# Kernel tuning notes

Hardware: AMD Instinct MI355X
Metric: run time of the kernel (lower is better)

## Reference

```python
import jax, jax.numpy as jnp
import numpy as np


def _gcn_conv(x, W, b, src, dst, n):
    # PyG GCNConv: add self-loops, symmetric normalization deg^{-1/2} A deg^{-1/2},
    # linear transform, scatter-add aggregation, bias.
    h = x @ W  # [N, H]
    # degree including self-loop (count of dst occurrences + 1)
    deg = jnp.zeros((n,), h.dtype).at[dst].add(1.0) + 1.0
    dinv = jax.lax.rsqrt(deg)  # deg^{-1/2}
    edge_norm = (dinv[src] * dinv[dst])[:, None]  # [E, 1]
    agg = jax.ops.segment_sum(h[src] * edge_norm, dst, num_segments=n)  # [N, H]
    # self-loop contribution: norm = dinv[i]*dinv[i]
    return agg + h * (dinv * dinv)[:, None] + b


def setup_inputs() -> dict:
    N, E, F_IN, HID, OUT = 100000, 1600000, 128, 128, 64
    key = jax.random.key(0)
    ks = jax.random.split(key, 8)
    x = jax.random.normal(ks[0], (N, F_IN), dtype=jnp.float32)
    edge_index = jax.random.randint(ks[1], (2, E), 0, N, dtype=jnp.int32)
    s1 = 1.0 / np.sqrt(F_IN)
    s2 = 1.0 / np.sqrt(HID)
    W1 = jax.random.uniform(ks[2], (F_IN, HID), jnp.float32, -s1, s1)
    b1 = jax.random.uniform(ks[3], (HID,), jnp.float32, -s1, s1)
    W2 = jax.random.uniform(ks[4], (HID, HID), jnp.float32, -s2, s2)
    b2 = jax.random.uniform(ks[5], (HID,), jnp.float32, -s2, s2)
    W_out = jax.random.uniform(ks[6], (HID, OUT), jnp.float32, -s2, s2)
    b_out = jax.random.uniform(ks[7], (OUT,), jnp.float32, -s2, s2)
    return {"x": x, "edge_index": edge_index, "W1": W1, "b1": b1,
            "W2": W2, "b2": b2, "W_out": W_out, "b_out": b_out}


def reference(x, edge_index, W1, b1, W2, b2, W_out, b_out):
    n = x.shape[0]
    src, dst = edge_index[0], edge_index[1]
    h = _gcn_conv(x, W1, b1, src, dst, n)
    h = jax.nn.relu(h)
    # F.dropout(training=self.training): identity in eval mode
    h = _gcn_conv(h, W2, b2, src, dst, n)
    h = jax.nn.relu(h)
    logits = h @ W_out + b_out
    return jax.nn.log_softmax(logits, axis=1)
```

## Files before the change

kernel.cpp:

```cpp
#include <hip/hip_runtime.h>
#include <hip/hip_bf16.h>


#define FEAT 128
#define OUTF 64
#define BSH 7
#define BNODES (1 << BSH)
#define SCHUNK_SH 12
#define SCHUNK (1 << SCHUNK_SH)
#define NREP 8
#define GDEPTH 16

typedef __attribute__((ext_vector_type(8))) short short8;
typedef __attribute__((ext_vector_type(4))) float f32x4;

__device__ __forceinline__ unsigned short bf16_rn(float f) {
    unsigned int u = __float_as_uint(f);
    u += 0x7FFFu + ((u >> 16) & 1u);
    return (unsigned short)(u >> 16);
}
__device__ __forceinline__ float bf16_lo(unsigned int u) { return __uint_as_float(u << 16); }
__device__ __forceinline__ float bf16_hi(unsigned int u) { return __uint_as_float(u & 0xFFFF0000u); }

__global__ __launch_bounds__(256) void bincount8_kernel(
        const int* __restrict__ dst, int* __restrict__ bcnt8, int E, int NB) {
    __shared__ int h[8192];
    int t = threadIdx.x;
    int nb8 = NB * NREP;
    for (int i = t; i < nb8; i += 256) h[i] = 0;
    __syncthreads();
    int stride = gridDim.x * 256;
    for (int e = blockIdx.x * 256 + t; e < E; e += stride) {
        int rep = (e >> SCHUNK_SH) & (NREP - 1);
        atomicAdd(&h[((dst[e] >> BSH) << 3) | rep], 1);
    }
    __syncthreads();
    for (int i = t; i < nb8; i += 256)
        if (h[i]) atomicAdd(&bcnt8[i], h[i]);
}

__global__ __launch_bounds__(1024) void bucket_scan8_kernel(
        const int* __restrict__ bcnt8, int* __restrict__ bcur8,
        int* __restrict__ bbase, int NB, int E) {
    int t = threadIdx.x;
    int nb8 = NB * NREP;
    int base = t * 8;
    int v[8];
    #pragma unroll
    for (int i = 0; i < 8; ++i) v[i] = (base + i < nb8) ? bcnt8[base + i] : 0;
    int local = 0;
    #pragma unroll
    for (int i = 0; i < 8; ++i) local += v[i];
    int lane = t & 63, wv = t >> 6;
    int x = local;
    #pragma unroll
    for (int o = 1; o < 64; o <<= 1) {
        int y = __shfl_up(x, o);
        if (lane >= o) x += y;
    }
    __shared__ int wsum[16];
    if (lane == 63) wsum[wv] = x;
    __syncthreads();
    int woff = 0;
    for (int i = 0; i < wv; ++i) woff += wsum[i];
    int run = woff + x - local;
    #pragma unroll
    for (int i = 0; i < 8; ++i) {
        int g = base + i;
        if (g < nb8) {
            bcur8[g] = run;
            if ((g & (NREP - 1)) == 0) bbase[g >> 3] = run;
        }
        run += v[i];
    }
    if (t == 0) bbase[NB] = E;
}

__global__ __launch_bounds__(256) void bin_scatter_kernel(
        const int* __restrict__ src, const int* __restrict__ dst,
        int* __restrict__ bcur8, unsigned int* __restrict__ staged,
        int E, int NB) {
    __shared__ int lcnt[1024];
    __shared__ int lbase[1024];
    int t = threadIdx.x;
    int rep = blockIdx.x & (NREP - 1);
    int e0 = blockIdx.x << SCHUNK_SH;
    int e1 = min(e0 + SCHUNK, E);
    for (int i = t; i < NB; i += 256) lcnt[i] = 0;
    __syncthreads();
    for (int e = e0 + t; e < e1; e += 256)
        atomicAdd(&lcnt[dst[e] >> BSH], 1);
    __syncthreads();
    for (int i = t; i < NB; i += 256) {
        int c = lcnt[i];
        lbase[i] = c ? atomicAdd(&bcur8[(i << 3) | rep], c) : 0;
        lcnt[i] = 0;
    }
    __syncthreads();
    for (int e = e0 + t; e < e1; e += 256) {
        int s = src[e], d = dst[e];
        int b = d >> BSH, dl = d & (BNODES - 1);
        int pos = lbase[b] + atomicAdd(&lcnt[b], 1);
        staged[pos] = (unsigned int)s | ((unsigned int)dl << 25);
    }
}

__global__ __launch_bounds__(256) void bucket_place_kernel(
        const unsigned int* __restrict__ staged, const int* __restrict__ bbase,
        int* __restrict__ row_ptr, float* __restrict__ dinv,
        int* __restrict__ csr_src, int N, int E) {
    int b = blockIdx.x;
    int t = threadIdx.x;
    int base = bbase[b], end = bbase[b + 1];
    __shared__ int cnt[BNODES];
    __shared__ int cur[BNODES];
    __shared__ int wsum2[2];
    if (t < BNODES) cnt[t] = 0;
    __syncthreads();
    for (int i = base + t; i < end; i += 256)
        atomicAdd(&cnt[staged[i] >> 25], 1);
    __syncthreads();

    bool act = t < BNODES;
    int v = act ? cnt[t] : 0;
    int lane = t & 63, wv = t >> 6;
    int x = v;
    #pragma unroll
    for (int o = 1; o < 64; o <<= 1) {
        int y = __shfl_up(x, o);
        if (lane >= o) x += y;
    }
    if (lane == 63 && wv == 0) wsum2[0] = x;
    __syncthreads();
    if (act) {
        int excl = x - v + (wv == 1 ? wsum2[0] : 0);
        int gnode = b * BNODES + t;
        int rp = base + excl;
        cur[t] = rp;
        if (gnode < N) {
            row_ptr[gnode] = rp;
            dinv[gnode] = rsqrtf((float)v + 1.0f);
        }
    }
    __syncthreads();
    for (int i = base + t; i < end; i += 256) {
        unsigned int u = staged[i];
        int dl = u >> 25;
        int p = atomicAdd(&cur[dl], 1);
        csr_src[p] = (int)(u & 0x1FFFFFFu);
    }
    if (b == 0 && t == 0) row_ptr[N] = E;
}

__global__ __launch_bounds__(256) void convw_kernel(
        const float* __restrict__ W1, const float* __restrict__ W2,
        const float* __restrict__ Wout,
        __hip_bfloat16* __restrict__ W1t, __hip_bfloat16* __restrict__ W2t,
        __hip_bfloat16* __restrict__ WoutT) {
    int idx = blockIdx.x * 256 + threadIdx.x;
    if (idx < 2 * FEAT * FEAT) {
        int which = idx >> 14;
        int r = idx & (FEAT * FEAT - 1);
        int n = r >> 7, k = r & 127;
        const float* W = which ? W2 : W1;
        unsigned short* Wt = (unsigned short*)(which ? W2t : W1t);
        Wt[r] = bf16_rn(W[k * FEAT + n]);
    } else if (idx < 2 * FEAT * FEAT + OUTF * FEAT) {
        int r = idx - 2 * FEAT * FEAT;
        int n = r >> 7, k = r & 127;
        ((unsigned short*)WoutT)[r] = bf16_rn(Wout[k * OUTF + n]);
    }
}

template <bool IN_FP32>
__global__ __launch_bounds__(256) void mfma_gemm_kernel(
        const void* __restrict__ Xv, const __hip_bfloat16* __restrict__ Wt,
        const float* __restrict__ dinv, __hip_bfloat16* __restrict__ Y, int N) {
    __shared__ short Ws[FEAT][136];
    int t = threadIdx.x;
    for (int i = t; i < FEAT * 16; i += 256) {
        int n = i >> 4, c = i & 15;
        *(uint4*)&Ws[n][c * 8] = *(const uint4*)((const unsigned short*)Wt + n * FEAT + c * 8);
    }
    __syncthreads();

    int wave = t >> 6, lane = t & 63;
    int m = lane & 15, quad = lane >> 4;
    int rbase = (blockIdx.x * 4 + wave) * 16;
    if (rbase >= N) return;
    int row = rbase + m;
    bool rok = row < N;

    f32x4 acc[8];
    #pragma unroll
    for (int nt = 0; nt < 8; ++nt) acc[nt] = (f32x4){0.f, 0.f, 0.f, 0.f};

    #pragma unroll
    for (int ks = 0; ks < 4; ++ks) {
        short8 a;
        if (IN_FP32) {
            const float* X = (const float*)Xv;
            float xs[8];
            if (rok) {
                float4 x0 = *(const float4*)(X + (size_t)row * FEAT + ks * 32 + quad * 8);
                float4 x1 = *(const float4*)(X + (size_t)row * FEAT + ks * 32 + quad * 8 + 4);
                xs[0] = x0.x; xs[1] = x0.y; xs[2] = x0.z; xs[3] = x0.w;
                xs[4] = x1.x; xs[5] = x1.y; xs[6] = x1.z; xs[7] = x1.w;
            } else {
                #pragma unroll
                for (int j = 0; j < 8; ++j) xs[j] = 0.f;
            }
            #pragma unroll
            for (int j = 0; j < 8; ++j) a[j] = (short)bf16_rn(xs[j]);
        } else {
            const unsigned short* X = (const unsigned short*)Xv;
            if (rok)
                a = *(const short8*)(X + (size_t)row * FEAT + ks * 32 + quad * 8);
            else {
                #pragma unroll
                for (int j = 0; j < 8; ++j) a[j] = 0;
            }
        }
        #pragma unroll
        for (int nt = 0; nt < 8; ++nt) {
            short8 bfr = *(const short8*)&Ws[nt * 16 + m][ks * 32 + quad * 8];
            acc[nt] = __builtin_amdgcn_mfma_f32_16x16x32_bf16(a, bfr, acc[nt], 0, 0, 0);
        }
    }

    float dr[4];
    #pragma unroll
    for (int r = 0; r < 4; ++r) {
        int ro = rbase + quad * 4 + r;
        dr[r] = (ro < N) ? dinv[ro] : 0.f;
    }
    unsigned short* Yo = (unsigned short*)Y;
    #pragma unroll
    for (int nt = 0; nt < 8; ++nt) {
        #pragma unroll
        for (int r = 0; r < 4; ++r) {
            int ro = rbase + quad * 4 + r;
            if (ro < N)
                Yo[(size_t)ro * FEAT + nt * 16 + m] = bf16_rn(acc[nt][r] * dr[r]);
        }
    }
}

template <int EPI>
__global__ __launch_bounds__(256, 4) void gather_fused_kernel(
        const int* __restrict__ row_ptr, const int* __restrict__ csr_src,
        const float* __restrict__ dinv, const __hip_bfloat16* __restrict__ Hs,
        const float* __restrict__ bias, const __hip_bfloat16* __restrict__ Wt,
        const float* __restrict__ bvec, void* __restrict__ outp, int N) {
    __shared__ short As[16][136];

    int t = threadIdx.x;
    int lane = t & 63;
    int wave = t >> 6;
    int grp = lane >> 4;
    int fl = lane & 15;
    int node = blockIdx.x * 16 + wave * 4 + grp;
    bool nok = node < N;
    int nd = nok ? node : 0;

    const char* Hb = (const char*)Hs;
    unsigned foff = (unsigned)fl << 4;

    uint4 hu = *(const uint4*)(Hb + (((unsigned)nd << 8) + foff));
    float di = dinv[nd];
    float4 b0 = ((const float4*)bias)[fl * 2];
    float4 b1 = ((const float4*)bias)[fl * 2 + 1];

    float acc[8];
    #pragma unroll
    for (int i = 0; i < 8; ++i) acc[i] = 0.f;

    int j = row_ptr[nd], end = row_ptr[nd + 1];

    for (; j + GDEPTH <= end; j += GDEPTH) {
        unsigned off[GDEPTH];
        #pragma unroll
        for (int k = 0; k < GDEPTH; ++k)
            off[k] = ((unsigned)csr_src[j + k] << 8) + foff;
        uint4 u[GDEPTH];
        #pragma unroll
        for (int k = 0; k < GDEPTH; ++k)
            u[k] = *(const uint4*)(Hb + off[k]);
        #pragma unroll
        for (int k = 0; k < GDEPTH; ++k) {
            acc[0] += bf16_lo(u[k].x); acc[1] += bf16_hi(u[k].x);
            acc[2] += bf16_lo(u[k].y); acc[3] += bf16_hi(u[k].y);
            acc[4] += bf16_lo(u[k].z); acc[5] += bf16_hi(u[k].z);
            acc[6] += bf16_lo(u[k].w); acc[7] += bf16_hi(u[k].w);
        }
    }
    if (j < end) {
        int mm = end - j;
        unsigned off[GDEPTH];
        #pragma unroll
        for (int k = 0; k < GDEPTH; ++k)
            off[k] = ((unsigned)csr_src[j + (k < mm ? k : 0)] << 8) + foff;
        uint4 u[GDEPTH];
        #pragma unroll
        for (int k = 0; k < GDEPTH; ++k)
            u[k] = *(const uint4*)(Hb + off[k]);
        #pragma unroll
        for (int k = 0; k < GDEPTH; ++k) {
            if (k < mm) {
                acc[0] += bf16_lo(u[k].x); acc[1] += bf16_hi(u[k].x);
                acc[2] += bf16_lo(u[k].y); acc[3] += bf16_hi(u[k].y);
                acc[4] += bf16_lo(u[k].z); acc[5] += bf16_hi(u[k].z);
                acc[6] += bf16_lo(u[k].w); acc[7] += bf16_hi(u[k].w);
            }
        }
    }

    acc[0] += bf16_lo(hu.x); acc[1] += bf16_hi(hu.x);
    acc[2] += bf16_lo(hu.y); acc[3] += bf16_hi(hu.y);
    acc[4] += bf16_lo(hu.z); acc[5] += bf16_hi(hu.z);
    acc[6] += bf16_lo(hu.w); acc[7] += bf16_hi(hu.w);

    float v0 = fmaxf(di * acc[0] + b0.x, 0.f);
    float v1 = fmaxf(di * acc[1] + b0.y, 0.f);
    float v2 = fmaxf(di * acc[2] + b0.z, 0.f);
    float v3 = fmaxf(di * acc[3] + b0.w, 0.f);
    float v4 = fmaxf(di * acc[4] + b1.x, 0.f);
    float v5 = fmaxf(di * acc[5] + b1.y, 0.f);
    float v6 = fmaxf(di * acc[6] + b1.z, 0.f);
    float v7 = fmaxf(di * acc[7] + b1.w, 0.f);

    uint4 o;
    o.x = (unsigned int)bf16_rn(v0) | ((unsigned int)bf16_rn(v1) << 16);
    o.y = (unsigned int)bf16_rn(v2) | ((unsigned int)bf16_rn(v3) << 16);
    o.z = (unsigned int)bf16_rn(v4) | ((unsigned int)bf16_rn(v5) << 16);
    o.w = (unsigned int)bf16_rn(v6) | ((unsigned int)bf16_rn(v7) << 16);

    *(uint4*)&As[wave * 4 + grp][fl * 8] = o;
    __syncthreads();

    int m = lane & 15, quad = lane >> 4;
    int rbase0 = blockIdx.x * 16;
    const unsigned short* Wu = (const unsigned short*)Wt;

    if (EPI == 1) {
        f32x4 acc2[2];
        #pragma unroll
        for (int n2 = 0; n2 < 2; ++n2) acc2[n2] = (f32x4){0.f, 0.f, 0.f, 0.f};
        #pragma unroll
        for (int ks = 0; ks < 4; ++ks) {
            short8 a = *(const short8*)&As[m][ks * 32 + quad * 8];
            #pragma unroll
            for (int n2 = 0; n2 < 2; ++n2) {
                int nt = wave * 2 + n2;
                short8 bfr = *(const short8*)(Wu + (nt * 16 + m) * FEAT + ks * 32 + quad * 8);
                acc2[n2] = __builtin_amdgcn_mfma_f32_16x16x32_bf16(a, bfr, acc2[n2], 0, 0, 0);
            }
        }
        unsigned short* Yo = (unsigned short*)outp;
        #pragma unroll
        for (int r = 0; r < 4; ++r) {
            int ro = rbase0 + quad * 4 + r;
            if (ro < N) {
                float dr = dinv[ro];
                #pragma unroll
                for (int n2 = 0; n2 < 2; ++n2)
                    Yo[(size_t)ro * FEAT + (wave * 2 + n2) * 16 + m] =
                        bf16_rn(acc2[n2][r] * dr);
            }
        }
    } else {
        if (wave == 0) {
            f32x4 acc4[4];
            #pragma unroll
            for (int nt = 0; nt < 4; ++nt) acc4[nt] = (f32x4){0.f, 0.f, 0.f, 0.f};
            #pragma unroll
            for (int ks = 0; ks < 4; ++ks) {
                short8 a = *(const short8*)&As[m][ks * 32 + quad * 8];
                #pragma unroll
                for (int nt = 0; nt < 4; ++nt) {
                    short8 bfr = *(const short8*)(Wu + (nt * 16 + m) * FEAT + ks * 32 + quad * 8);
                    acc4[nt] = __builtin_amdgcn_mfma_f32_16x16x32_bf16(a, bfr, acc4[nt], 0, 0, 0);
                }
            }
            float bj[4];
            #pragma unroll
            for (int nt = 0; nt < 4; ++nt) bj[nt] = bvec[nt * 16 + m];
            float* out = (float*)outp;
            #pragma unroll
            for (int r = 0; r < 4; ++r) {
                int ro = rbase0 + quad * 4 + r;
                if (ro >= N) continue;
                float w0 = acc4[0][r] + bj[0];
                float w1 = acc4[1][r] + bj[1];
                float w2 = acc4[2][r] + bj[2];
                float w3 = acc4[3][r] + bj[3];
                float mx = fmaxf(fmaxf(w0, w1), fmaxf(w2, w3));
                #pragma unroll
                for (int os = 1; os <= 8; os <<= 1) mx = fmaxf(mx, __shfl_xor(mx, os));
                float s = __expf(w0 - mx) + __expf(w1 - mx) + __expf(w2 - mx) + __expf(w3 - mx);
                #pragma unroll
                for (int os = 1; os <= 8; os <<= 1) s += __shfl_xor(s, os);
                float ls = mx + __logf(s);
                float* op = out + (size_t)ro * OUTF + m;
                op[0]  = w0 - ls;
                op[16] = w1 - ls;
                op[32] = w2 - ls;
                op[48] = w3 - ls;
            }
        }
    }
}

extern "C" void kernel_launch(void* const* d_in, const int* in_sizes, int n_in,
                              void* d_out, int out_size, void* d_ws, size_t ws_size,
                              hipStream_t stream) {
    const float* x    = (const float*)d_in[0];
    const int*   ei   = (const int*)  d_in[1];
    const float* W1   = (const float*)d_in[2];
    const float* b1   = (const float*)d_in[3];
    const float* W2   = (const float*)d_in[4];
    const float* b2   = (const float*)d_in[5];
    const float* Wout = (const float*)d_in[6];
    const float* bout = (const float*)d_in[7];
    float* out = (float*)d_out;

    int N = in_sizes[0] / FEAT;
    int E = in_sizes[1] / 2;
    const int* srcp = ei;
    const int* dstp = ei + E;
    int NB = (N + BNODES - 1) >> BSH;

    char* ws = (char*)d_ws;
    __hip_bfloat16* Bh   = (__hip_bfloat16*)ws;
    __hip_bfloat16* Ba   = Bh + (size_t)N * FEAT;
    __hip_bfloat16* W1t  = Ba + (size_t)N * FEAT;
    __hip_bfloat16* W2t  = W1t + FEAT * FEAT;
    __hip_bfloat16* WoutT = W2t + FEAT * FEAT;
    float* dinv    = (float*)(WoutT + OUTF * FEAT);
    int*   rowp    = (int*)(dinv + N);
    int*   bcnt8   = rowp + N + 1;
    int*   bcur8   = bcnt8 + 8192;
    int*   bbase   = bcur8 + 8192;
    unsigned int* staged = (unsigned int*)(bbase + 1032);
    int*   csrsrc  = (int*)(staged + E);

    hipMemsetAsync(bcnt8, 0, (size_t)NB * NREP * sizeof(int), stream);
    bincount8_kernel<<<256, 256, 0, stream>>>(dstp, bcnt8, E, NB);
    bucket_scan8_kernel<<<1, 1024, 0, stream>>>(bcnt8, bcur8, bbase, NB, E);
    bin_scatter_kernel<<<(E + SCHUNK - 1) / SCHUNK, 256, 0, stream>>>(
        srcp, dstp, bcur8, staged, E, NB);
    bucket_place_kernel<<<NB, 256, 0, stream>>>(staged, bbase, rowp, dinv, csrsrc, N, E);
    convw_kernel<<<(2 * FEAT * FEAT + OUTF * FEAT + 255) / 256, 256, 0, stream>>>(
        W1, W2, Wout, W1t, W2t, WoutT);

    int ggrid = (N + 63) / 64;
    int agrid = (N + 15) / 16;

    mfma_gemm_kernel<true><<<ggrid, 256, 0, stream>>>(x, W1t, dinv, Bh, N);

    gather_fused_kernel<1><<<agrid, 256, 0, stream>>>(
        rowp, csrsrc, dinv, Bh, b1, W2t, nullptr, Ba, N);

    gather_fused_kernel<2><<<agrid, 256, 0, stream>>>(
        rowp, csrsrc, dinv, Ba, b2, WoutT, bout, out, N);
}
```

Before: 325.3 us.

## Gather rows directly in MFMA A-fragment layout, dropping LDS staging and barrier

The fused gather kernel now has each wave own 16 nodes, with each lane accumulating a node's features in exactly the layout the MFMA A operand needs. This removes the shared-memory tile, the block barrier, and the idle waves in the log-softmax epilogue. The cost is that the 16 lanes in a quad now walk 16 different nodes' edge lists in lockstep, so warp divergence comes from degree variance. Gather depth drops from 16 to 3 rows (12 loads each), and register pressure rises with the 4x8 accumulators.

```diff
diff --git a/kernel.cpp b/kernel.cpp
--- a/kernel.cpp
+++ b/kernel.cpp
@@ -9,7 +9,7 @@
 #define SCHUNK_SH 12
 #define SCHUNK (1 << SCHUNK_SH)
 #define NREP 8
-#define GDEPTH 16
+#define GD 3
 
 typedef __attribute__((ext_vector_type(8))) short short8;
 typedef __attribute__((ext_vector_type(4))) float f32x4;
@@ -252,161 +252,170 @@
         const float* __restrict__ dinv, const __hip_bfloat16* __restrict__ Hs,
         const float* __restrict__ bias, const __hip_bfloat16* __restrict__ Wt,
         const float* __restrict__ bvec, void* __restrict__ outp, int N) {
-    __shared__ short As[16][136];
-
     int t = threadIdx.x;
     int lane = t & 63;
     int wave = t >> 6;
-    int grp = lane >> 4;
-    int fl = lane & 15;
-    int node = blockIdx.x * 16 + wave * 4 + grp;
+    int m = lane & 15;
+    int quad = lane >> 4;
+    int wbase = (blockIdx.x * 4 + wave) * 16;
+    if (wbase >= N) return;
+    int node = wbase + m;
     bool nok = node < N;
     int nd = nok ? node : 0;
 
     const char* Hb = (const char*)Hs;
-    unsigned foff = (unsigned)fl << 4;
-
-    uint4 hu = *(const uint4*)(Hb + (((unsigned)nd << 8) + foff));
-    float di = dinv[nd];
-    float4 b0 = ((const float4*)bias)[fl * 2];
-    float4 b1 = ((const float4*)bias)[fl * 2 + 1];
-
-    float acc[8];
-    #pragma unroll
-    for (int i = 0; i < 8; ++i) acc[i] = 0.f;
+    unsigned coff = (unsigned)quad << 4;
+
+    float acc[4][8];
+    #pragma unroll
+    for (int a = 0; a < 4; ++a)
+        #pragma unroll
+        for (int c = 0; c < 8; ++c) acc[a][c] = 0.f;
 
     int j = row_ptr[nd], end = row_ptr[nd + 1];
 
-    for (; j + GDEPTH <= end; j += GDEPTH) {
-        unsigned off[GDEPTH];
-        #pragma unroll
-        for (int k = 0; k < GDEPTH; ++k)
-            off[k] = ((unsigned)csr_src[j + k] << 8) + foff;
-        uint4 u[GDEPTH];
-        #pragma unroll
-        for (int k = 0; k < GDEPTH; ++k)
-            u[k] = *(const uint4*)(Hb + off[k]);
-        #pragma unroll
-        for (int k = 0; k < GDEPTH; ++k) {
-            acc[0] += bf16_lo(u[k].x); acc[1] += bf16_hi(u[k].x);
-            acc[2] += bf16_lo(u[k].y); acc[3] += bf16_hi(u[k].y);
-            acc[4] += bf16_lo(u[k].z); acc[5] += bf16_hi(u[k].z);
-            acc[6] += bf16_lo(u[k].w); acc[7] += bf16_hi(u[k].w);
-        }
+    for (; j + GD <= end; j += GD) {
+        unsigned off[GD];
+        #pragma unroll
+        for (int k = 0; k < GD; ++k)
+            off[k] = ((unsigned)csr_src[j + k] << 8) + coff;
+        uint4 u[GD][4];
+        #pragma unroll
+        for (int k = 0; k < GD; ++k)
+            #pragma unroll
+            for (int ks = 0; ks < 4; ++ks)
+                u[k][ks] = *(const uint4*)(Hb + off[k] + ks * 64);
+        #pragma unroll
+        for (int k = 0; k < GD; ++k)
+            #pragma unroll
+            for (int ks = 0; ks < 4; ++ks) {
+                acc[ks][0] += bf16_lo(u[k][ks].x); acc[ks][1] += bf16_hi(u[k][ks].x);
+                acc[ks][2] += bf16_lo(u[k][ks].y); acc[ks][3] += bf16_hi(u[k][ks].y);
+                acc[ks][4] += bf16_lo(u[k][ks].z); acc[ks][5] += bf16_hi(u[k][ks].z);
+                acc[ks][6] += bf16_lo(u[k][ks].w); acc[ks][7] += bf16_hi(u[k][ks].w);
+            }
     }
     if (j < end) {
         int mm = end - j;
-        unsigned off[GDEPTH];
-        #pragma unroll
-        for (int k = 0; k < GDEPTH; ++k)
-            off[k] = ((unsigned)csr_src[j + (k < mm ? k : 0)] << 8) + foff;
-        uint4 u[GDEPTH];
-        #pragma unroll
-        for (int k = 0; k < GDEPTH; ++k)
-            u[k] = *(const uint4*)(Hb + off[k]);
-        #pragma unroll
-        for (int k = 0; k < GDEPTH; ++k) {
+        unsigned off[GD];
+        #pragma unroll
+        for (int k = 0; k < GD; ++k)
+            off[k] = ((unsigned)csr_src[j + (k < mm ? k : 0)] << 8) + coff;
+        uint4 u[GD][4];
+        #pragma unroll
+        for (int k = 0; k < GD; ++k)
+            #pragma unroll
+            for (int ks = 0; ks < 4; ++ks)
+                u[k][ks] = *(const uint4*)(Hb + off[k] + ks * 64);
+        #pragma unroll
+        for (int k = 0; k < GD; ++k) {
             if (k < mm) {
-                acc[0] += bf16_lo(u[k].x); acc[1] += bf16_hi(u[k].x);
-                acc[2] += bf16_lo(u[k].y); acc[3] += bf16_hi(u[k].y);
-                acc[4] += bf16_lo(u[k].z); acc[5] += bf16_hi(u[k].z);
-                acc[6] += bf16_lo(u[k].w); acc[7] += bf16_hi(u[k].w);
-            }
-        }
-    }
-
-    acc[0] += bf16_lo(hu.x); acc[1] += bf16_hi(hu.x);
-    acc[2] += bf16_lo(hu.y); acc[3] += bf16_hi(hu.y);
-    acc[4] += bf16_lo(hu.z); acc[5] += bf16_hi(hu.z);
-    acc[6] += bf16_lo(hu.w); acc[7] += bf16_hi(hu.w);
-
-    float v0 = fmaxf(di * acc[0] + b0.x, 0.f);
-    float v1 = fmaxf(di * acc[1] + b0.y, 0.f);
-    float v2 = fmaxf(di * acc[2] + b0.z, 0.f);
-    float v3 = fmaxf(di * acc[3] + b0.w, 0.f);
-    float v4 = fmaxf(di * acc[4] + b1.x, 0.f);
-    float v5 = fmaxf(di * acc[5] + b1.y, 0.f);
-    float v6 = fmaxf(di * acc[6] + b1.z, 0.f);
-    float v7 = fmaxf(di * acc[7] + b1.w, 0.f);
-
-    uint4 o;
-    o.x = (unsigned int)bf16_rn(v0) | ((unsigned int)bf16_rn(v1) << 16);
-    o.y = (unsigned int)bf16_rn(v2) | ((unsigned int)bf16_rn(v3) << 16);
-    o.z = (unsigned int)bf16_rn(v4) | ((unsigned int)bf16_rn(v5) << 16);
-    o.w = (unsigned int)bf16_rn(v6) | ((unsigned int)bf16_rn(v7) << 16);
-
-    *(uint4*)&As[wave * 4 + grp][fl * 8] = o;
-    __syncthreads();
-
-    int m = lane & 15, quad = lane >> 4;
-    int rbase0 = blockIdx.x * 16;
+                #pragma unroll
+                for (int ks = 0; ks < 4; ++ks) {
+                    acc[ks][0] += bf16_lo(u[k][ks].x); acc[ks][1] += bf16_hi(u[k][ks].x);
+                    acc[ks][2] += bf16_lo(u[k][ks].y); acc[ks][3] += bf16_hi(u[k][ks].y);
+                    acc[ks][4] += bf16_lo(u[k][ks].z); acc[ks][5] += bf16_hi(u[k][ks].z);
+                    acc[ks][6] += bf16_lo(u[k][ks].w); acc[ks][7] += bf16_hi(u[k][ks].w);
+                }
+            }
+        }
+    }
+    {
+        unsigned off0 = ((unsigned)nd << 8) + coff;
+        uint4 su[4];
+        #pragma unroll
+        for (int ks = 0; ks < 4; ++ks)
+            su[ks] = *(const uint4*)(Hb + off0 + ks * 64);
+        #pragma unroll
+        for (int ks = 0; ks < 4; ++ks) {
+            acc[ks][0] += bf16_lo(su[ks].x); acc[ks][1] += bf16_hi(su[ks].x);
+            acc[ks][2] += bf16_lo(su[ks].y); acc[ks][3] += bf16_hi(su[ks].y);
+            acc[ks][4] += bf16_lo(su[ks].z); acc[ks][5] += bf16_hi(su[ks].z);
+            acc[ks][6] += bf16_lo(su[ks].w); acc[ks][7] += bf16_hi(su[ks].w);
+        }
+    }
+
+    float di = dinv[nd];
+    short8 afr[4];
+    #pragma unroll
+    for (int ks = 0; ks < 4; ++ks) {
+        float4 bb0 = ((const float4*)bias)[ks * 8 + quad * 2];
+        float4 bb1 = ((const float4*)bias)[ks * 8 + quad * 2 + 1];
+        float w0 = fmaxf(di * acc[ks][0] + bb0.x, 0.f);
+        float w1 = fmaxf(di * acc[ks][1] + bb0.y, 0.f);
+        float w2 = fmaxf(di * acc[ks][2] + bb0.z, 0.f);
+        float w3 = fmaxf(di * acc[ks][3] + bb0.w, 0.f);
+        float w4 = fmaxf(di * acc[ks][4] + bb1.x, 0.f);
+        float w5 = fmaxf(di * acc[ks][5] + bb1.y, 0.f);
+        float w6 = fmaxf(di * acc[ks][6] + bb1.z, 0.f);
+        float w7 = fmaxf(di * acc[ks][7] + bb1.w, 0.f);
+        afr[ks][0] = (short)bf16_rn(w0); afr[ks][1] = (short)bf16_rn(w1);
+        afr[ks][2] = (short)bf16_rn(w2); afr[ks][3] = (short)bf16_rn(w3);
+        afr[ks][4] = (short)bf16_rn(w4); afr[ks][5] = (short)bf16_rn(w5);
+        afr[ks][6] = (short)bf16_rn(w6); afr[ks][7] = (short)bf16_rn(w7);
+    }
+
     const unsigned short* Wu = (const unsigned short*)Wt;
 
     if (EPI == 1) {
-        f32x4 acc2[2];
-        #pragma unroll
-        for (int n2 = 0; n2 < 2; ++n2) acc2[n2] = (f32x4){0.f, 0.f, 0.f, 0.f};
+        float dr[4];
+        #pragma unroll
+        for (int r = 0; r < 4; ++r) {
+            int ro = wbase + quad * 4 + r;
+            dr[r] = (ro < N) ? dinv[ro] : 0.f;
+        }
+        unsigned short* Yo = (unsigned short*)outp;
+        #pragma unroll
+        for (int nt = 0; nt < 8; ++nt) {
+            f32x4 d = (f32x4){0.f, 0.f, 0.f, 0.f};
+            #pragma unroll
+            for (int ks = 0; ks < 4; ++ks) {
+                short8 bfr = *(const short8*)(Wu + (nt * 16 + m) * FEAT + ks * 32 + quad * 8);
+                d = __builtin_amdgcn_mfma_f32_16x16x32_bf16(afr[ks], bfr, d, 0, 0, 0);
+            }
+            #pragma unroll
+            for (int r = 0; r < 4; ++r) {
+                int ro = wbase + quad * 4 + r;
+                if (ro < N)
+                    Yo[(size_t)ro * FEAT + nt * 16 + m] = bf16_rn(d[r] * dr[r]);
+            }
+        }
+    } else {
+        f32x4 acc4[4];
+        #pragma unroll
+        for (int nt = 0; nt < 4; ++nt) acc4[nt] = (f32x4){0.f, 0.f, 0.f, 0.f};
         #pragma unroll
         for (int ks = 0; ks < 4; ++ks) {
-            short8 a = *(const short8*)&As[m][ks * 32 + quad * 8];
-            #pragma unroll
-            for (int n2 = 0; n2 < 2; ++n2) {
-                int nt = wave * 2 + n2;
+            #pragma unroll
+            for (int nt = 0; nt < 4; ++nt) {
                 short8 bfr = *(const short8*)(Wu + (nt * 16 + m) * FEAT + ks * 32 + quad * 8);
-                acc2[n2] = __builtin_amdgcn_mfma_f32_16x16x32_bf16(a, bfr, acc2[n2], 0, 0, 0);
-            }
-        }
-        unsigned short* Yo = (unsigned short*)outp;
+                acc4[nt] = __builtin_amdgcn_mfma_f32_16x16x32_bf16(afr[ks], bfr, acc4[nt], 0, 0, 0);
+            }
+        }
+        float bj[4];
+        #pragma unroll
+        for (int nt = 0; nt < 4; ++nt) bj[nt] = bvec[nt * 16 + m];
+        float* out = (float*)outp;
         #pragma unroll
         for (int r = 0; r < 4; ++r) {
-            int ro = rbase0 + quad * 4 + r;
-            if (ro < N) {
-                float dr = dinv[ro];
-                #pragma unroll
-                for (int n2 = 0; n2 < 2; ++n2)
-                    Yo[(size_t)ro * FEAT + (wave * 2 + n2) * 16 + m] =
-                        bf16_rn(acc2[n2][r] * dr);
-            }
-        }
-    } else {
-        if (wave == 0) {
-            f32x4 acc4[4];
-            #pragma unroll
-            for (int nt = 0; nt < 4; ++nt) acc4[nt] = (f32x4){0.f, 0.f, 0.f, 0.f};
-            #pragma unroll
-            for (int ks = 0; ks < 4; ++ks) {
-                short8 a = *(const short8*)&As[m][ks * 32 + quad * 8];
-                #pragma unroll
-                for (int nt = 0; nt < 4; ++nt) {
-                    short8 bfr = *(const short8*)(Wu + (nt * 16 + m) * FEAT + ks * 32 + quad * 8);
-                    acc4[nt] = __builtin_amdgcn_mfma_f32_16x16x32_bf16(a, bfr, acc4[nt], 0, 0, 0);
-                }
-            }
-            float bj[4];
-            #pragma unroll
-            for (int nt = 0; nt < 4; ++nt) bj[nt] = bvec[nt * 16 + m];
-            float* out = (float*)outp;
-            #pragma unroll
-            for (int r = 0; r < 4; ++r) {
-                int ro = rbase0 + quad * 4 + r;
-                if (ro >= N) continue;
-                float w0 = acc4[0][r] + bj[0];
-                float w1 = acc4[1][r] + bj[1];
-                float w2 = acc4[2][r] + bj[2];
-                float w3 = acc4[3][r] + bj[3];
-                float mx = fmaxf(fmaxf(w0, w1), fmaxf(w2, w3));
-                #pragma unroll
-                for (int os = 1; os <= 8; os <<= 1) mx = fmaxf(mx, __shfl_xor(mx, os));
-                float s = __expf(w0 - mx) + __expf(w1 - mx) + __expf(w2 - mx) + __expf(w3 - mx);
-                #pragma unroll
-                for (int os = 1; os <= 8; os <<= 1) s += __shfl_xor(s, os);
-                float ls = mx + __logf(s);
-                float* op = out + (size_t)ro * OUTF + m;
-                op[0]  = w0 - ls;
-                op[16] = w1 - ls;
-                op[32] = w2 - ls;
-                op[48] = w3 - ls;
-            }
+            int ro = wbase + quad * 4 + r;
+            if (ro >= N) continue;
+            float w0 = acc4[0][r] + bj[0];
+            float w1 = acc4[1][r] + bj[1];
+            float w2 = acc4[2][r] + bj[2];
+            float w3 = acc4[3][r] + bj[3];
+            float mx = fmaxf(fmaxf(w0, w1), fmaxf(w2, w3));
+            #pragma unroll
+            for (int os = 1; os <= 8; os <<= 1) mx = fmaxf(mx, __shfl_xor(mx, os));
+            float s = __expf(w0 - mx) + __expf(w1 - mx) + __expf(w2 - mx) + __expf(w3 - mx);
+            #pragma unroll
+            for (int os = 1; os <= 8; os <<= 1) s += __shfl_xor(s, os);
+            float ls = mx + __logf(s);
+            float* op = out + (size_t)ro * OUTF + m;
+            op[0]  = w0 - ls;
+            op[16] = w1 - ls;
+            op[32] = w2 - ls;
+            op[48] = w3 - ls;
         }
     }
 }
@@ -454,13 +463,12 @@
         W1, W2, Wout, W1t, W2t, WoutT);
 
     int ggrid = (N + 63) / 64;
-    int agrid = (N + 15) / 16;
 
     mfma_gemm_kernel<true><<<ggrid, 256, 0, stream>>>(x, W1t, dinv, Bh, N);
 
-    gather_fused_kernel<1><<<agrid, 256, 0, stream>>>(
+    gather_fused_kernel<1><<<ggrid, 256, 0, stream>>>(
         rowp, csrsrc, dinv, Bh, b1, W2t, nullptr, Ba, N);
 
-    gather_fused_kernel<2><<<agrid, 256, 0, stream>>>(
+    gather_fused_kernel<2><<<ggrid, 256, 0, stream>>>(
         rowp, csrsrc, dinv, Ba, b2, WoutT, bout, out, N);
 }
```

Result: slower. 377.2 us (+15.9%).
